# Performance work log

Measured on AMD Instinct MI355X. Metric: run time of the kernel, lower is better.

Reference implementation:

```python
import jax, jax.numpy as jnp
import numpy as np

C = 128          # feature channels
N = 1_048_576    # octree nodes at depth 6 (divisible by 8)
M = 262_144      # full parent node count at depth 5 (incl. empty nodes)


def setup_inputs() -> dict:
    key = jax.random.key(0)
    k1, k2, k3 = jax.random.split(key, 3)
    data = jax.random.normal(k1, (C, N), dtype=jnp.float32)
    idx = jax.random.randint(k2, (M,), 0, N // 8, dtype=jnp.int32)
    empty = jax.random.uniform(k3, (M,)) < 0.5
    child_idx = jnp.where(empty, jnp.int32(-1), idx)  # -1 => empty (zero pad)
    return {"data": data, "child_idx": child_idx}


def reference(data, child_idx):
    # octree_max_pool: every 8 consecutive sibling nodes -> 1 parent value
    c, n = data.shape
    grouped = data.reshape(c, n // 8, 8)          # [C, N/8, 8]
    pooled = grouped.max(axis=-1)                  # [C, N/8]
    # octree_pad: scatter pooled non-empty parents into full parent node list,
    # zero-filling empty nodes (child_idx == -1).
    safe = jnp.clip(child_idx, 0, None)            # safe gather index
    out = jnp.where(child_idx[None, :] >= 0, pooled[:, safe], jnp.float32(0))
    return out                                     # [C, M]
```

## Files before the change

kernel.cpp:

```cpp
#include <hip/hip_runtime.h>


#define CH 128

__global__ __launch_bounds__(256) void pool_t_kernel(
    const float* __restrict__ data,
    float* __restrict__ pooled_t,
    int n,
    int gpc)
{
    int t  = threadIdx.x;
    int gl = t >> 5;
    int cq = t & 31;
    int g  = blockIdx.x * 8 + gl;
    if (g >= gpc) return;
    int c0 = cq * 4;

    const float* base = data + (size_t)g * 8;
    float v[4];
    #pragma unroll
    for (int k = 0; k < 4; ++k) {
        const float4* p = (const float4*)(base + (size_t)(c0 + k) * n);
        float4 a = p[0];
        float4 b = p[1];
        v[k] = fmaxf(fmaxf(fmaxf(a.x, a.y), fmaxf(a.z, a.w)),
                     fmaxf(fmaxf(b.x, b.y), fmaxf(b.z, b.w)));
    }
    *(float4*)(pooled_t + (size_t)g * CH + c0) = make_float4(v[0], v[1], v[2], v[3]);
}

__global__ __launch_bounds__(256) void pad_t_kernel(
    const float* __restrict__ pooled_t,
    const int* __restrict__ child_idx,
    float* __restrict__ out,
    int m_total)
{
    int m = blockIdx.x * 256 + threadIdx.x;
    if (m >= m_total) return;
    int idx = child_idx[m];
    int c0 = blockIdx.y * 32;

    if (idx < 0) {
        #pragma unroll
        for (int k = 0; k < 32; ++k)
            out[(size_t)(c0 + k) * m_total + m] = 0.0f;
        return;
    }

    const float4* rec = (const float4*)(pooled_t + (size_t)idx * CH + c0);
    float4 v[8];
    #pragma unroll
    for (int k = 0; k < 8; ++k) v[k] = rec[k];
    #pragma unroll
    for (int k = 0; k < 8; ++k) {
        out[(size_t)(c0 + 4 * k + 0) * m_total + m] = v[k].x;
        out[(size_t)(c0 + 4 * k + 1) * m_total + m] = v[k].y;
        out[(size_t)(c0 + 4 * k + 2) * m_total + m] = v[k].z;
        out[(size_t)(c0 + 4 * k + 3) * m_total + m] = v[k].w;
    }
}

__global__ __launch_bounds__(256) void fused_kernel(
    const float* __restrict__ data,
    const int* __restrict__ child_idx,
    float* __restrict__ out,
    int n, int m_total)
{
    int m = blockIdx.x * 256 + threadIdx.x;
    if (m >= m_total) return;
    int idx = child_idx[m];
    int c0 = blockIdx.y * 8;
    if (idx < 0) {
        #pragma unroll
        for (int cc = 0; cc < 8; ++cc)
            out[(size_t)(c0 + cc) * m_total + m] = 0.0f;
        return;
    }
    size_t base = (size_t)idx * 8;
    #pragma unroll
    for (int cc = 0; cc < 8; ++cc) {
        const float4* p = (const float4*)(data + (size_t)(c0 + cc) * n + base);
        float4 a = p[0];
        float4 b = p[1];
        out[(size_t)(c0 + cc) * m_total + m] =
            fmaxf(fmaxf(fmaxf(a.x, a.y), fmaxf(a.z, a.w)),
                  fmaxf(fmaxf(b.x, b.y), fmaxf(b.z, b.w)));
    }
}

extern "C" void kernel_launch(void* const* d_in, const int* in_sizes, int n_in,
                              void* d_out, int out_size, void* d_ws, size_t ws_size,
                              hipStream_t stream) {
    const float* data      = (const float*)d_in[0];
    const int*   child_idx = (const int*)d_in[1];
    float*       out       = (float*)d_out;

    int n   = in_sizes[0] / CH;
    int m   = in_sizes[1];
    int gpc = n / 8;
    size_t pooled_bytes = (size_t)gpc * CH * sizeof(float);

    if (ws_size >= pooled_bytes) {
        float* pooled_t = (float*)d_ws;
        dim3 b1(256), g1((gpc + 7) / 8);
        hipLaunchKernelGGL(pool_t_kernel, g1, b1, 0, stream, data, pooled_t, n, gpc);
        dim3 b2(256), g2((m + 255) / 256, 4);
        hipLaunchKernelGGL(pad_t_kernel, g2, b2, 0, stream, pooled_t, child_idx, out, m);
    } else {
        dim3 b(256), g((m + 255) / 256, CH / 8);
        hipLaunchKernelGGL(fused_kernel, g, b, 0, stream, data, child_idx, out, n, m);
    }
}
```

Measured before the change: 802.1 us.

## Coalesce pooling reads via LDS-tiled transpose and make padding branchless

New measurement: 762.6 us. 4.9% less time.

```diff
diff --git a/kernel.cpp b/kernel.cpp
--- a/kernel.cpp
+++ b/kernel.cpp
@@ -1,7 +1,8 @@
 #include <hip/hip_runtime.h>
 
 
-#define CH 128
+#define CH  128
+#define GPB 64
 
 __global__ __launch_bounds__(256) void pool_t_kernel(
     const float* __restrict__ data,
@@ -9,24 +10,46 @@
     int n,
     int gpc)
 {
-    int t  = threadIdx.x;
-    int gl = t >> 5;
-    int cq = t & 31;
-    int g  = blockIdx.x * 8 + gl;
-    if (g >= gpc) return;
-    int c0 = cq * 4;
+    __shared__ float tile[GPB][CH + 1];
 
-    const float* base = data + (size_t)g * 8;
-    float v[4];
-    #pragma unroll
-    for (int k = 0; k < 4; ++k) {
-        const float4* p = (const float4*)(base + (size_t)(c0 + k) * n);
-        float4 a = p[0];
-        float4 b = p[1];
-        v[k] = fmaxf(fmaxf(fmaxf(a.x, a.y), fmaxf(a.z, a.w)),
-                     fmaxf(fmaxf(b.x, b.y), fmaxf(b.z, b.w)));
+    int t    = threadIdx.x;
+    int g0   = blockIdx.x * GPB;
+    int lane = t & 127;
+    int rhf  = t >> 7;
+    int gl   = lane >> 1;
+    int h    = lane & 1;
+
+    if (g0 + GPB <= gpc) {
+        const float* base = data + (size_t)g0 * 8;
+        #pragma unroll 4
+        for (int r = 0; r < CH; r += 2) {
+            int row = r + rhf;
+            float4 a = *(const float4*)(base + (size_t)row * n + lane * 4);
+            float m = fmaxf(fmaxf(a.x, a.y), fmaxf(a.z, a.w));
+            m = fmaxf(m, __shfl_xor(m, 1));
+            if (h == 0) tile[gl][row] = m;
+        }
+        __syncthreads();
+
+        int cq = t & 31;
+        int r0 = t >> 5;
+        #pragma unroll
+        for (int w = 0; w < 8; ++w) {
+            int rec = w * 8 + r0;
+            float4 v = make_float4(tile[rec][cq * 4 + 0], tile[rec][cq * 4 + 1],
+                                   tile[rec][cq * 4 + 2], tile[rec][cq * 4 + 3]);
+            *(float4*)(pooled_t + (size_t)(g0 + rec) * CH + cq * 4) = v;
+        }
+    } else {
+        for (int g = g0 + t; g < gpc; g += 256) {
+            for (int c = 0; c < CH; ++c) {
+                const float* p = data + (size_t)c * n + (size_t)g * 8;
+                float m = p[0];
+                for (int k = 1; k < 8; ++k) m = fmaxf(m, p[k]);
+                pooled_t[(size_t)g * CH + c] = m;
+            }
+        }
     }
-    *(float4*)(pooled_t + (size_t)g * CH + c0) = make_float4(v[0], v[1], v[2], v[3]);
 }
 
 __global__ __launch_bounds__(256) void pad_t_kernel(
@@ -37,26 +60,20 @@
 {
     int m = blockIdx.x * 256 + threadIdx.x;
     if (m >= m_total) return;
-    int idx = child_idx[m];
-    int c0 = blockIdx.y * 32;
+    int idx  = child_idx[m];
+    bool live = (idx >= 0);
+    int rec  = live ? idx : 0;
+    int c0   = blockIdx.y * 64;
 
-    if (idx < 0) {
-        #pragma unroll
-        for (int k = 0; k < 32; ++k)
-            out[(size_t)(c0 + k) * m_total + m] = 0.0f;
-        return;
-    }
-
-    const float4* rec = (const float4*)(pooled_t + (size_t)idx * CH + c0);
-    float4 v[8];
+    const float4* recp = (const float4*)(pooled_t + (size_t)rec * CH + c0);
     #pragma unroll
-    for (int k = 0; k < 8; ++k) v[k] = rec[k];
-    #pragma unroll
-    for (int k = 0; k < 8; ++k) {
-        out[(size_t)(c0 + 4 * k + 0) * m_total + m] = v[k].x;
-        out[(size_t)(c0 + 4 * k + 1) * m_total + m] = v[k].y;
-        out[(size_t)(c0 + 4 * k + 2) * m_total + m] = v[k].z;
-        out[(size_t)(c0 + 4 * k + 3) * m_total + m] = v[k].w;
+    for (int k = 0; k < 16; ++k) {
+        float4 v = recp[k];
+        size_t c = (size_t)(c0 + 4 * k);
+        out[(c + 0) * m_total + m] = live ? v.x : 0.0f;
+        out[(c + 1) * m_total + m] = live ? v.y : 0.0f;
+        out[(c + 2) * m_total + m] = live ? v.z : 0.0f;
+        out[(c + 3) * m_total + m] = live ? v.w : 0.0f;
     }
 }
 
@@ -100,11 +117,11 @@
     int gpc = n / 8;
     size_t pooled_bytes = (size_t)gpc * CH * sizeof(float);
 
-    if (ws_size >= pooled_bytes) {
+    if (ws_size >= pooled_bytes && (n % 8) == 0) {
         float* pooled_t = (float*)d_ws;
-        dim3 b1(256), g1((gpc + 7) / 8);
+        dim3 b1(256), g1((gpc + GPB - 1) / GPB);
         hipLaunchKernelGGL(pool_t_kernel, g1, b1, 0, stream, data, pooled_t, n, gpc);
-        dim3 b2(256), g2((m + 255) / 256, 4);
+        dim3 b2(256), g2((m + 255) / 256, 2);
         hipLaunchKernelGGL(pad_t_kernel, g2, b2, 0, stream, pooled_t, child_idx, out, m);
     } else {
         dim3 b(256), g((m + 255) / 256, CH / 8);
```
